# Kernel tuning notes

Measured on AMD Instinct MI355X. Metric: run time of the kernel, lower is better.

The kernel has to match this reference:

```python
import jax, jax.numpy as jnp
import numpy as np

W_DIST = 1.0
W_ANGLE = 1.0
EPS = 1e-12


def setup_inputs() -> dict:
    key = jax.random.key(0)
    k1, k2, k3 = jax.random.split(key, 3)
    B, C = 384, 512
    return {
        "feat_s": jax.random.normal(k1, (B, C), dtype=jnp.float32),
        "feat_t": jax.random.normal(k2, (B, C), dtype=jnp.float32),
        "labels": jax.random.randint(k3, (B,), 0, C, dtype=jnp.int64),
    }


def _pdist(feat):
    # Euclidean pairwise distances with zeroed diagonal (matches RKD.pdist).
    sq = jnp.sum(feat * feat, axis=1)                      # [B]
    prod = feat @ feat.T                                   # [B,B]
    d = jnp.clip(sq[None, :] + sq[:, None] - 2.0 * prod, EPS, None)
    d = jnp.sqrt(d)
    B = feat.shape[0]
    return d * (1.0 - jnp.eye(B, dtype=feat.dtype))


def _norm_pdist(feat):
    d = _pdist(feat)
    pos = d > 0
    mean_pos = jnp.sum(jnp.where(pos, d, 0.0)) / jnp.maximum(jnp.sum(pos), 1)
    return d / mean_pos


def _smooth_l1(x, y):
    a = jnp.abs(x - y)
    return jnp.mean(jnp.where(a < 1.0, 0.5 * a * a, a - 0.5))


def _angle_gram(feat):
    # vd[i, j] = feat[j] - feat[i], normalized along feature dim (F.normalize eps=1e-12)
    vd = feat[None, :, :] - feat[:, None, :]               # [B,B,C]
    nrm = jnp.sqrt(jnp.sum(vd * vd, axis=2, keepdims=True))
    vd = vd / jnp.maximum(nrm, EPS)
    return jnp.einsum('bic,bjc->bij', vd, vd)              # [B,B,B]


def _rkd(feat_s, feat_t):
    dist_loss = _smooth_l1(_norm_pdist(feat_s), _norm_pdist(feat_t))
    angle_loss = _smooth_l1(_angle_gram(feat_s), _angle_gram(feat_t))
    return W_DIST * dist_loss + W_ANGLE * angle_loss


def reference(feat_s, feat_t, labels):
    # hard CE loss (mean reduction)
    logp = jax.nn.log_softmax(feat_s, axis=-1)
    hard_loss = -jnp.mean(logp[jnp.arange(feat_s.shape[0]), labels])
    # soft RKD loss; teacher detached as in the torch code
    soft_loss = _rkd(feat_s, jax.lax.stop_gradient(feat_t))
    return hard_loss + soft_loss
```

## Files before the change

### kernel.cpp

```cpp
#include <hip/hip_runtime.h>
#include <hip/hip_bf16.h>
#include <math.h>

#define B 384
#define C 512
#define NPAIR (B * B)
#define NOFF  (B * (B - 1))

#define T16  24
#define UP16 300
#define T64  6
#define UP64 21
#define NBG  48
#define NANG (UP64 * NBG)

#define HARD_OFF 0
#define DSUM_OFF 384
#define ANG_OFF  984
#define DIST_OFF 1992
#define SQS_OFF  2016
#define SQT_OFF  2400
#define PS_OFF   2816
#define PT_OFF   (PS_OFF + NPAIR)

typedef __attribute__((ext_vector_type(8))) short short8;
typedef __attribute__((ext_vector_type(4))) float floatx4;

__device__ __forceinline__ float blk_sum(float v, float* s4, int t) {
#pragma unroll
  for (int off = 32; off > 0; off >>= 1) v += __shfl_down(v, off, 64);
  if ((t & 63) == 0) s4[t >> 6] = v;
  __syncthreads();
  float r = s4[0] + s4[1] + s4[2] + s4[3];
  __syncthreads();
  return r;
}

__device__ __forceinline__ short bfc(float x) {
  __hip_bfloat16 h = __float2bfloat16(x);
  return __builtin_bit_cast(short, h);
}

__global__ __launch_bounds__(256, 4) void k_pre(const float* __restrict__ fs,
                                                const float* __restrict__ ft,
                                                const int* __restrict__ lab,
                                                float* __restrict__ ws) {
  int t = threadIdx.x;
  if (blockIdx.x < 96) {
    int wv = t >> 6, lane = t & 63;
    int r = blockIdx.x * 4 + wv;
    const float* xs = fs + r * C;
    const float* xt = ft + r * C;
    float4 a0 = *(const float4*)&xs[lane * 8];
    float4 a1 = *(const float4*)&xs[lane * 8 + 4];
    float4 b0 = *(const float4*)&xt[lane * 8];
    float4 b1 = *(const float4*)&xt[lane * 8 + 4];
    float m = fmaxf(fmaxf(fmaxf(a0.x, a0.y), fmaxf(a0.z, a0.w)),
                    fmaxf(fmaxf(a1.x, a1.y), fmaxf(a1.z, a1.w)));
#pragma unroll
    for (int off = 32; off > 0; off >>= 1) m = fmaxf(m, __shfl_down(m, off, 64));
    m = __shfl(m, 0, 64);
    float es = expf(a0.x - m) + expf(a0.y - m) + expf(a0.z - m) + expf(a0.w - m) +
               expf(a1.x - m) + expf(a1.y - m) + expf(a1.z - m) + expf(a1.w - m);
    float ss = a0.x * a0.x + a0.y * a0.y + a0.z * a0.z + a0.w * a0.w +
               a1.x * a1.x + a1.y * a1.y + a1.z * a1.z + a1.w * a1.w;
    float st = b0.x * b0.x + b0.y * b0.y + b0.z * b0.z + b0.w * b0.w +
               b1.x * b1.x + b1.y * b1.y + b1.z * b1.z + b1.w * b1.w;
#pragma unroll
    for (int off = 32; off > 0; off >>= 1) {
      es += __shfl_down(es, off, 64);
      ss += __shfl_down(ss, off, 64);
      st += __shfl_down(st, off, 64);
    }
    if (lane == 0) {
      ws[SQS_OFF + r] = ss;
      ws[SQT_OFF + r] = st;
      ws[HARD_OFF + r] = m + logf(es) - xs[lab[r]];
    }
  } else {
    int w = t >> 6, lane = t & 63;
    int g = (blockIdx.x - 96) * 4 + w;
    int tensor = (g >= UP16) ? 1 : 0;
    int uu = g - tensor * UP16;
    int ti = 0;
    while (uu >= T16 - ti) { uu -= T16 - ti; ++ti; }
    int tj = ti + uu;
    const float* F = tensor ? ft : fs;
    float* P = ws + (tensor ? PT_OFF : PS_OFF);
    int i0 = ti * 16, j0 = tj * 16;
    int r = lane & 15, q = lane >> 4;
    const float* arow = F + (i0 + r) * C + q * 8;
    const float* brow = F + (j0 + r) * C + q * 8;
    floatx4 acc = {0.f, 0.f, 0.f, 0.f};
    float sqa = 0.f, sqb = 0.f;
#pragma unroll
    for (int ks = 0; ks < 16; ++ks) {
      float4 al = *(const float4*)(arow + ks * 32);
      float4 ah = *(const float4*)(arow + ks * 32 + 4);
      float4 bl = *(const float4*)(brow + ks * 32);
      float4 bh = *(const float4*)(brow + ks * 32 + 4);
      sqa += al.x * al.x + al.y * al.y + al.z * al.z + al.w * al.w +
             ah.x * ah.x + ah.y * ah.y + ah.z * ah.z + ah.w * ah.w;
      sqb += bl.x * bl.x + bl.y * bl.y + bl.z * bl.z + bl.w * bl.w +
             bh.x * bh.x + bh.y * bh.y + bh.z * bh.z + bh.w * bh.w;
      short8 a, b;
      a[0] = bfc(al.x); a[1] = bfc(al.y); a[2] = bfc(al.z); a[3] = bfc(al.w);
      a[4] = bfc(ah.x); a[5] = bfc(ah.y); a[6] = bfc(ah.z); a[7] = bfc(ah.w);
      b[0] = bfc(bl.x); b[1] = bfc(bl.y); b[2] = bfc(bl.z); b[3] = bfc(bl.w);
      b[4] = bfc(bh.x); b[5] = bfc(bh.y); b[6] = bfc(bh.z); b[7] = bfc(bh.w);
      acc = __builtin_amdgcn_mfma_f32_16x16x32_bf16(a, b, acc, 0, 0, 0);
    }
    sqa += __shfl_xor(sqa, 16, 64); sqa += __shfl_xor(sqa, 32, 64);
    sqb += __shfl_xor(sqb, 16, 64); sqb += __shfl_xor(sqb, 32, 64);
    int col = lane & 15;
    int j = j0 + col;
    float sqj = __shfl(sqb, col, 64);
    float dsum = 0.f;
#pragma unroll
    for (int reg = 0; reg < 4; ++reg) {
      int ii = q * 4 + reg;
      int i = i0 + ii;
      float sqi = __shfl(sqa, ii, 64);
      float p = acc[reg];
      P[i * B + j] = p;
      P[j * B + i] = p;
      float d2 = sqi + sqj - 2.f * p;
      float d = sqrtf(fmaxf(d2, 1e-12f));
      float wgt = (ti < tj) ? 2.f : ((i < j) ? 2.f : 0.f);
      dsum = fmaf(wgt, d, dsum);
    }
#pragma unroll
    for (int off = 32; off > 0; off >>= 1) dsum += __shfl_down(dsum, off, 64);
    if (lane == 0) ws[DSUM_OFF + g] = dsum;
  }
}

#define BCH 8
__global__ __launch_bounds__(256, 3) void k_angle(float* __restrict__ ws) {
  const float* Ps = ws + PS_OFF;
  const float* Pt = ws + PT_OFF;
  const float* sqs = ws + SQS_OFF;
  const float* sqt = ws + SQT_OFF;
  int uu = blockIdx.x;
  int ti = 0;
  while (uu >= T64 - ti) { uu -= T64 - ti; ++ti; }
  int tj = ti + uu;
  int i0 = ti * 64, j0 = tj * 64;
  bool diag = (ti == tj);
  int b0 = blockIdx.y * BCH;
  int t = threadIdx.x;
  int ty = t >> 4, tx = t & 15;

  __shared__ float4 sI4[BCH][64];
  __shared__ float4 sJ4[BCH][64];
  __shared__ float s4[4];

  float ps[4][4], pt[4][4];
#pragma unroll
  for (int r = 0; r < 4; ++r) {
    float4 v = *(const float4*)&Ps[(i0 + ty * 4 + r) * B + j0 + tx * 4];
    ps[r][0] = v.x; ps[r][1] = v.y; ps[r][2] = v.z; ps[r][3] = v.w;
    v = *(const float4*)&Pt[(i0 + ty * 4 + r) * B + j0 + tx * 4];
    pt[r][0] = v.x; pt[r][1] = v.y; pt[r][2] = v.z; pt[r][3] = v.w;
  }

  for (int idx = t; idx < BCH * 128; idx += 256) {
    int b = idx >> 7, p = idx & 127;
    int bb = b0 + b;
    int col = (p < 64) ? (i0 + p) : (j0 + p - 64);
    float pvs = Ps[bb * B + col];
    float pvt = Pt[bb * B + col];
    float pbbs = Ps[bb * B + bb];
    float pbbt = Pt[bb * B + bb];
    float d2s = sqs[bb] + sqs[col] - 2.f * pvs;
    float d2t = sqt[bb] + sqt[col] - 2.f * pvt;
    float us = (col == bb) ? 0.f : rsqrtf(fmaxf(d2s, 1e-24f));
    float ut = (col == bb) ? 0.f : rsqrtf(fmaxf(d2t, 1e-24f));
    float4 pk;
    pk.x = us;
    pk.y = us * (pvs - 0.5f * pbbs);
    pk.z = ut;
    pk.w = ut * (pvt - 0.5f * pbbt);
    if (p < 64) sI4[b][p] = pk; else sJ4[b][p - 64] = pk;
  }
  __syncthreads();

  float acc = 0.f;
  float4 vi[4], vj[4], nvi[4], nvj[4];
#pragma unroll
  for (int r = 0; r < 4; ++r) {
    vi[r] = sI4[0][ty * 4 + r];
    vj[r] = sJ4[0][tx * 4 + r];
  }
#pragma unroll
  for (int b = 0; b < BCH; ++b) {
    if (b + 1 < BCH) {
#pragma unroll
      for (int r = 0; r < 4; ++r) {
        nvi[r] = sI4[b + 1][ty * 4 + r];
        nvj[r] = sJ4[b + 1][tx * 4 + r];
      }
    }
#pragma unroll
    for (int r = 0; r < 4; ++r) {
#pragma unroll
      for (int c = 0; c < 4; ++c) {
        float f1s = fmaf(vi[r].x, ps[r][c], -vi[r].y);
        float gs = fmaf(vj[c].x, f1s, -(vi[r].x * vj[c].y));
        float f1t = fmaf(vi[r].z, pt[r][c], -vi[r].w);
        float gt = fmaf(vj[c].z, f1t, -(vi[r].z * vj[c].w));
        float a = fabsf(gs - gt);
        if (diag) a = (ty * 4 + r < tx * 4 + c) ? a : 0.f;
        float mm = fminf(a, 1.f);
        acc = fmaf(mm, fmaf(-0.5f, mm, a), acc);
      }
    }
#pragma unroll
    for (int r = 0; r < 4; ++r) { vi[r] = nvi[r]; vj[r] = nvj[r]; }
  }

  float asum = blk_sum(acc, s4, t);
  if (t == 0) ws[ANG_OFF + blockIdx.y * UP64 + blockIdx.x] = asum;

  if (blockIdx.y == 0) {
    float ssum = 0.f, tsum = 0.f;
    for (int i = t; i < UP16; i += 256) ssum += ws[DSUM_OFF + i];
    for (int i = t; i < UP16; i += 256) tsum += ws[DSUM_OFF + UP16 + i];
    ssum = blk_sum(ssum, s4, t);
    tsum = blk_sum(tsum, s4, t);
    float inv_ms = (float)NOFF / ssum;
    float inv_mt = (float)NOFF / tsum;
    float sqsi[4], sqti[4], sqsj[4], sqtj[4];
#pragma unroll
    for (int r = 0; r < 4; ++r) {
      sqsi[r] = sqs[i0 + ty * 4 + r];
      sqti[r] = sqt[i0 + ty * 4 + r];
      sqsj[r] = sqs[j0 + tx * 4 + r];
      sqtj[r] = sqt[j0 + tx * 4 + r];
    }
    float dacc = 0.f;
#pragma unroll
    for (int r = 0; r < 4; ++r)
#pragma unroll
      for (int c = 0; c < 4; ++c) {
        float d2s = sqsi[r] + sqsj[c] - 2.f * ps[r][c];
        float d2t = sqti[r] + sqtj[c] - 2.f * pt[r][c];
        float dsv = sqrtf(fmaxf(d2s, 1e-12f)) * inv_ms;
        float dtv = sqrtf(fmaxf(d2t, 1e-12f)) * inv_mt;
        float a = fabsf(dsv - dtv);
        if (diag) a = (ty * 4 + r < tx * 4 + c) ? a : 0.f;
        float mm = fminf(a, 1.f);
        dacc = fmaf(mm, fmaf(-0.5f, mm, a), dacc);
      }
    float dsum2 = blk_sum(dacc, s4, t);
    if (t == 0) ws[DIST_OFF + blockIdx.x] = dsum2;
  }
}

__global__ __launch_bounds__(256) void k_final(const float* __restrict__ ws,
                                               float* __restrict__ out) {
  __shared__ float s4[4];
  int t = threadIdx.x;
  float h = 0.f;
  for (int i = t; i < B; i += 256) h += ws[HARD_OFF + i];
  float a = 0.f;
  for (int i = t; i < NANG; i += 256) a += ws[ANG_OFF + i];
  float d = 0.f;
  for (int i = t; i < UP64; i += 256) d += ws[DIST_OFF + i];
  h = blk_sum(h, s4, t);
  a = blk_sum(a, s4, t);
  d = blk_sum(d, s4, t);
  if (t == 0)
    out[0] = h * (1.f / (float)B) + 2.f * d * (1.f / (float)NPAIR) +
             2.f * a * (1.f / 56623104.f);
}

extern "C" void kernel_launch(void* const* d_in, const int* in_sizes, int n_in,
                              void* d_out, int out_size, void* d_ws, size_t ws_size,
                              hipStream_t stream) {
  (void)in_sizes; (void)n_in; (void)out_size; (void)ws_size;
  const float* fs = (const float*)d_in[0];
  const float* ft = (const float*)d_in[1];
  const int* lab = (const int*)d_in[2];
  float* ws = (float*)d_ws;
  float* out = (float*)d_out;

  k_pre<<<246, 256, 0, stream>>>(fs, ft, lab, ws);
  k_angle<<<dim3(UP64, NBG), 256, 0, stream>>>(ws);
  k_final<<<1, 256, 0, stream>>>(ws, out);
}
```

Baseline: 81.87 us.

## Shrink angle kernel to single-wave 32x32 tiles with separate distance blocks

The angle kernel now uses 64-thread single-wavefront blocks over 32x32 upper-triangle tiles (78 tiles) instead of 256-thread blocks over 64x64 tiles. Block reductions become wave shuffles with no __syncthreads. The distance-loss work moves from blockIdx.y==0 into an extra row of dedicated blocks. Shared-memory rows are padded so the float4 reads avoid bank conflicts. This aims to raise block count and balance load and to remove barrier overhead, at the cost of more redundant per-block row/column preprocessing and smaller tiles.

```diff
diff --git a/kernel.cpp b/kernel.cpp
--- a/kernel.cpp
+++ b/kernel.cpp
@@ -9,18 +9,19 @@
 
 #define T16  24
 #define UP16 300
-#define T64  6
-#define UP64 21
+#define T32  12
+#define UP32 78
+#define BCH  8
 #define NBG  48
-#define NANG (UP64 * NBG)
+#define NANGB (UP32 * NBG)
 
 #define HARD_OFF 0
 #define DSUM_OFF 384
 #define ANG_OFF  984
-#define DIST_OFF 1992
-#define SQS_OFF  2016
-#define SQT_OFF  2400
-#define PS_OFF   2816
+#define DIST_OFF 4728
+#define SQS_OFF  4816
+#define SQT_OFF  5200
+#define PS_OFF   5632
 #define PT_OFF   (PS_OFF + NPAIR)
 
 typedef __attribute__((ext_vector_type(8))) short short8;
@@ -135,25 +136,22 @@
   }
 }
 
-#define BCH 8
-__global__ __launch_bounds__(256, 3) void k_angle(float* __restrict__ ws) {
+__global__ __launch_bounds__(64, 4) void k_angle(float* __restrict__ ws) {
   const float* Ps = ws + PS_OFF;
   const float* Pt = ws + PT_OFF;
   const float* sqs = ws + SQS_OFF;
   const float* sqt = ws + SQT_OFF;
   int uu = blockIdx.x;
   int ti = 0;
-  while (uu >= T64 - ti) { uu -= T64 - ti; ++ti; }
+  while (uu >= T32 - ti) { uu -= T32 - ti; ++ti; }
   int tj = ti + uu;
-  int i0 = ti * 64, j0 = tj * 64;
+  int i0 = ti * 32, j0 = tj * 32;
   bool diag = (ti == tj);
-  int b0 = blockIdx.y * BCH;
-  int t = threadIdx.x;
-  int ty = t >> 4, tx = t & 15;
-
-  __shared__ float4 sI4[BCH][64];
-  __shared__ float4 sJ4[BCH][64];
-  __shared__ float s4[4];
+  int lane = threadIdx.x;
+  int ty = lane >> 3, tx = lane & 7;
+
+  __shared__ float4 sI4[BCH][36];
+  __shared__ float4 sJ4[BCH][36];
 
   float ps[4][4], pt[4][4];
 #pragma unroll
@@ -164,16 +162,56 @@
     pt[r][0] = v.x; pt[r][1] = v.y; pt[r][2] = v.z; pt[r][3] = v.w;
   }
 
-  for (int idx = t; idx < BCH * 128; idx += 256) {
-    int b = idx >> 7, p = idx & 127;
+  if (blockIdx.y == NBG) {
+    float dsums = 0.f, dsumt = 0.f;
+    for (int i = lane; i < UP16; i += 64) dsums += ws[DSUM_OFF + i];
+    for (int i = lane; i < UP16; i += 64) dsumt += ws[DSUM_OFF + UP16 + i];
+#pragma unroll
+    for (int off = 32; off > 0; off >>= 1) {
+      dsums += __shfl_down(dsums, off, 64);
+      dsumt += __shfl_down(dsumt, off, 64);
+    }
+    dsums = __shfl(dsums, 0, 64);
+    dsumt = __shfl(dsumt, 0, 64);
+    float inv_ms = (float)NOFF / dsums;
+    float inv_mt = (float)NOFF / dsumt;
+    float dacc = 0.f;
+#pragma unroll
+    for (int r = 0; r < 4; ++r) {
+      float sqsi = sqs[i0 + ty * 4 + r];
+      float sqti = sqt[i0 + ty * 4 + r];
+#pragma unroll
+      for (int c = 0; c < 4; ++c) {
+        float d2s = sqsi + sqs[j0 + tx * 4 + c] - 2.f * ps[r][c];
+        float d2t = sqti + sqt[j0 + tx * 4 + c] - 2.f * pt[r][c];
+        float dsv = sqrtf(fmaxf(d2s, 1e-12f)) * inv_ms;
+        float dtv = sqrtf(fmaxf(d2t, 1e-12f)) * inv_mt;
+        float a = fabsf(dsv - dtv);
+        if (diag) a = (ty * 4 + r < tx * 4 + c) ? a : 0.f;
+        float mm = fminf(a, 1.f);
+        dacc = fmaf(mm, fmaf(-0.5f, mm, a), dacc);
+      }
+    }
+#pragma unroll
+    for (int off = 32; off > 0; off >>= 1) dacc += __shfl_down(dacc, off, 64);
+    if (lane == 0) ws[DIST_OFF + blockIdx.x] = dacc;
+    return;
+  }
+
+  int b0 = blockIdx.y * BCH;
+  int k = lane & 31;
+  int col = (lane < 32) ? (i0 + k) : (j0 + k);
+  int slot = k + (k >> 3);
+  float sqcs = sqs[col], sqct = sqt[col];
+#pragma unroll
+  for (int b = 0; b < BCH; ++b) {
     int bb = b0 + b;
-    int col = (p < 64) ? (i0 + p) : (j0 + p - 64);
     float pvs = Ps[bb * B + col];
     float pvt = Pt[bb * B + col];
     float pbbs = Ps[bb * B + bb];
     float pbbt = Pt[bb * B + bb];
-    float d2s = sqs[bb] + sqs[col] - 2.f * pvs;
-    float d2t = sqt[bb] + sqt[col] - 2.f * pvt;
+    float d2s = sqs[bb] + sqcs - 2.f * pvs;
+    float d2t = sqt[bb] + sqct - 2.f * pvt;
     float us = (col == bb) ? 0.f : rsqrtf(fmaxf(d2s, 1e-24f));
     float ut = (col == bb) ? 0.f : rsqrtf(fmaxf(d2t, 1e-24f));
     float4 pk;
@@ -181,26 +219,18 @@
     pk.y = us * (pvs - 0.5f * pbbs);
     pk.z = ut;
     pk.w = ut * (pvt - 0.5f * pbbt);
-    if (p < 64) sI4[b][p] = pk; else sJ4[b][p - 64] = pk;
+    if (lane < 32) sI4[b][slot] = pk; else sJ4[b][slot] = pk;
   }
   __syncthreads();
 
   float acc = 0.f;
-  float4 vi[4], vj[4], nvi[4], nvj[4];
-#pragma unroll
-  for (int r = 0; r < 4; ++r) {
-    vi[r] = sI4[0][ty * 4 + r];
-    vj[r] = sJ4[0][tx * 4 + r];
-  }
 #pragma unroll
   for (int b = 0; b < BCH; ++b) {
-    if (b + 1 < BCH) {
-#pragma unroll
-      for (int r = 0; r < 4; ++r) {
-        nvi[r] = sI4[b + 1][ty * 4 + r];
-        nvj[r] = sJ4[b + 1][tx * 4 + r];
-      }
-    }
+    float4 vi[4], vj[4];
+#pragma unroll
+    for (int r = 0; r < 4; ++r) vi[r] = sI4[b][ty * 4 + r + (ty >> 1)];
+#pragma unroll
+    for (int c = 0; c < 4; ++c) vj[c] = sJ4[b][tx * 4 + c + (tx >> 1)];
 #pragma unroll
     for (int r = 0; r < 4; ++r) {
 #pragma unroll
@@ -215,46 +245,10 @@
         acc = fmaf(mm, fmaf(-0.5f, mm, a), acc);
       }
     }
-#pragma unroll
-    for (int r = 0; r < 4; ++r) { vi[r] = nvi[r]; vj[r] = nvj[r]; }
-  }
-
-  float asum = blk_sum(acc, s4, t);
-  if (t == 0) ws[ANG_OFF + blockIdx.y * UP64 + blockIdx.x] = asum;
-
-  if (blockIdx.y == 0) {
-    float ssum = 0.f, tsum = 0.f;
-    for (int i = t; i < UP16; i += 256) ssum += ws[DSUM_OFF + i];
-    for (int i = t; i < UP16; i += 256) tsum += ws[DSUM_OFF + UP16 + i];
-    ssum = blk_sum(ssum, s4, t);
-    tsum = blk_sum(tsum, s4, t);
-    float inv_ms = (float)NOFF / ssum;
-    float inv_mt = (float)NOFF / tsum;
-    float sqsi[4], sqti[4], sqsj[4], sqtj[4];
-#pragma unroll
-    for (int r = 0; r < 4; ++r) {
-      sqsi[r] = sqs[i0 + ty * 4 + r];
-      sqti[r] = sqt[i0 + ty * 4 + r];
-      sqsj[r] = sqs[j0 + tx * 4 + r];
-      sqtj[r] = sqt[j0 + tx * 4 + r];
-    }
-    float dacc = 0.f;
-#pragma unroll
-    for (int r = 0; r < 4; ++r)
-#pragma unroll
-      for (int c = 0; c < 4; ++c) {
-        float d2s = sqsi[r] + sqsj[c] - 2.f * ps[r][c];
-        float d2t = sqti[r] + sqtj[c] - 2.f * pt[r][c];
-        float dsv = sqrtf(fmaxf(d2s, 1e-12f)) * inv_ms;
-        float dtv = sqrtf(fmaxf(d2t, 1e-12f)) * inv_mt;
-        float a = fabsf(dsv - dtv);
-        if (diag) a = (ty * 4 + r < tx * 4 + c) ? a : 0.f;
-        float mm = fminf(a, 1.f);
-        dacc = fmaf(mm, fmaf(-0.5f, mm, a), dacc);
-      }
-    float dsum2 = blk_sum(dacc, s4, t);
-    if (t == 0) ws[DIST_OFF + blockIdx.x] = dsum2;
-  }
+  }
+#pragma unroll
+  for (int off = 32; off > 0; off >>= 1) acc += __shfl_down(acc, off, 64);
+  if (lane == 0) ws[ANG_OFF + blockIdx.y * UP32 + blockIdx.x] = acc;
 }
 
 __global__ __launch_bounds__(256) void k_final(const float* __restrict__ ws,
@@ -264,9 +258,9 @@
   float h = 0.f;
   for (int i = t; i < B; i += 256) h += ws[HARD_OFF + i];
   float a = 0.f;
-  for (int i = t; i < NANG; i += 256) a += ws[ANG_OFF + i];
+  for (int i = t; i < NANGB; i += 256) a += ws[ANG_OFF + i];
   float d = 0.f;
-  for (int i = t; i < UP64; i += 256) d += ws[DIST_OFF + i];
+  for (int i = t; i < UP32; i += 256) d += ws[DIST_OFF + i];
   h = blk_sum(h, s4, t);
   a = blk_sum(a, s4, t);
   d = blk_sum(d, s4, t);
@@ -286,6 +280,6 @@
   float* out = (float*)d_out;
 
   k_pre<<<246, 256, 0, stream>>>(fs, ft, lab, ws);
-  k_angle<<<dim3(UP64, NBG), 256, 0, stream>>>(ws);
+  k_angle<<<dim3(UP32, NBG + 1), 64, 0, stream>>>(ws);
   k_final<<<1, 256, 0, stream>>>(ws, out);
 }
```

Result: slower. 84.75 us (+3.5%).
